# Kernel tuning notes

Hardware: AMD Instinct MI355X
Metric: run time of the kernel (lower is better)

The kernel has to match this reference:

```python
import jax, jax.numpy as jnp
import numpy as np

COMPRESSION = 2

def setup_inputs() -> dict:
    key = jax.random.key(0)
    k = jax.random.split(key, 5)
    B, H, W, C, Ci = 8, 56, 56, 256, 128
    return {
        "x": jax.random.normal(k[0], (B, H, W, C), dtype=jnp.float32),
        "w_theta": jax.random.normal(k[1], (C, Ci), dtype=jnp.float32) * (2.0 / C) ** 0.5,
        "w_phi": jax.random.normal(k[2], (C, Ci), dtype=jnp.float32) * (2.0 / C) ** 0.5,
        "w_g": jax.random.normal(k[3], (C, Ci), dtype=jnp.float32) * (2.0 / C) ** 0.5,
        "w_final": jax.random.normal(k[4], (Ci, C), dtype=jnp.float32) * (2.0 / Ci) ** 0.5,
    }

def _maxpool1d(z, pool):
    # z: [B, N, Ci]; non-overlapping max pool along N (Keras MaxPool1D default stride=pool)
    B, N, Ci = z.shape
    return z[:, : (N // pool) * pool].reshape(B, N // pool, pool, Ci).max(axis=2)

def reference(x, w_theta, w_phi, w_g, w_final):
    B, H, W, C = x.shape
    Ci = w_theta.shape[1]
    N = H * W
    xf = x.reshape(B, N, C)
    # 1x1 convs == per-position matmuls
    theta = xf @ w_theta                      # [B, N, Ci]
    phi = _maxpool1d(xf @ w_phi, COMPRESSION)  # [B, N/2, Ci]
    g = _maxpool1d(xf @ w_g, COMPRESSION)      # [B, N/2, Ci]
    f = jnp.einsum('bnc,bmc->bnm', theta, phi)  # [B, N, N/2]
    f = jax.nn.softmax(f, axis=-1)
    y = jnp.einsum('bnm,bmc->bnc', f, g)        # [B, N, Ci]
    z = y @ w_final                              # [B, N, C]
    return x + z.reshape(B, H, W, C)
```

## Files before the change

### kernel.cpp

```cpp
#include <hip/hip_runtime.h>

typedef _Float16 f16x8 __attribute__((ext_vector_type(8)));
typedef short s16x4 __attribute__((ext_vector_type(4)));
typedef float f32x4 __attribute__((ext_vector_type(4)));

#define MFMA_K32(a, b, c) __builtin_amdgcn_mfma_f32_16x16x32_f16(a, b, c, 0, 0, 0)
#define MFMA_BF(a, b, c)  __builtin_amdgcn_mfma_f32_16x16x16bf16_1k(a, b, c, 0, 0, 0)


__device__ __forceinline__ f16x8 ld8f(const float* __restrict__ p) {
    f32x4 a = *(const f32x4*)p;
    f32x4 b = *(const f32x4*)(p + 4);
    f16x8 r;
    r[0] = (_Float16)a[0]; r[1] = (_Float16)a[1];
    r[2] = (_Float16)a[2]; r[3] = (_Float16)a[3];
    r[4] = (_Float16)b[0]; r[5] = (_Float16)b[1];
    r[6] = (_Float16)b[2]; r[7] = (_Float16)b[3];
    return r;
}
__device__ __forceinline__ unsigned f2bf_rne(float f) {
    unsigned u = __float_as_uint(f);
    return (u + 0x7FFFu + ((u >> 16) & 1u)) >> 16;
}
__device__ __forceinline__ int bfpack_rtz(float lo, float hi) {
    return (int)((__float_as_uint(hi) & 0xFFFF0000u) | (__float_as_uint(lo) >> 16));
}

__global__ void k_prep(const float* __restrict__ wt, const float* __restrict__ wp,
                       const float* __restrict__ wg, const float* __restrict__ wf,
                       _Float16* __restrict__ wt_f, _Float16* __restrict__ wf_f) {
    int i = blockIdx.x * 256 + threadIdx.x;
    int w = i >> 15, idx = i & 32767;
    if (w < 3) {
        const float* src = (w == 0) ? wt : (w == 1) ? wp : wg;
        int k = idx >> 7, n = idx & 127;
        int ct = n >> 4, tt = n & 15, kc = k >> 5, qq = (k >> 3) & 3, jj = k & 7;
        wt_f[((w * 8 + ct) * 8 + kc) * 512 + (qq * 16 + tt) * 8 + jj] = (_Float16)src[idx];
    } else {
        int k = idx >> 8, n = idx & 255;
        int cb = n >> 7, ct = (n >> 4) & 7, tt = n & 15;
        int kc = k >> 5, qq = (k >> 3) & 3, jj = k & 7;
        wf_f[((cb * 8 + ct) * 4 + kc) * 512 + (qq * 16 + tt) * 8 + jj] = (_Float16)wf[idx];
    }
}

__global__ __launch_bounds__(128) void k_proj(
    const float* __restrict__ x,
    const _Float16* __restrict__ wt_f,
    _Float16* __restrict__ theta_f,
    _Float16* __restrict__ phi_f,
    short* __restrict__ g_f)
{
    const int r0   = blockIdx.x * 32;
    const int wave = threadIdx.x >> 6;
    const int lane = threadIdx.x & 63;
    const int q = lane >> 4, t = lane & 15;

    const int mrow = r0 + wave * 16 + t;
    f16x8 af[8];
#pragma unroll
    for (int kc = 0; kc < 8; ++kc)
        af[kc] = ld8f(x + mrow * 256 + kc * 32 + q * 8);

    const f32x4 zero = {0.f, 0.f, 0.f, 0.f};
    f32x4 acc[3][8];
#pragma unroll
    for (int w = 0; w < 3; ++w)
#pragma unroll
        for (int ct = 0; ct < 8; ++ct) acc[w][ct] = zero;

#pragma unroll
    for (int w = 0; w < 3; ++w)
#pragma unroll
        for (int ct = 0; ct < 8; ++ct) {
            const _Float16* Wc = wt_f + ((w * 8 + ct) * 8) * 512 + lane * 8;
#pragma unroll
            for (int kc = 0; kc < 8; ++kc)
                acc[w][ct] = MFMA_K32(af[kc], *(const f16x8*)(Wc + kc * 512), acc[w][ct]);
        }

    _Float16* tb = theta_f + (blockIdx.x * 2 + wave) * 2048;
#pragma unroll
    for (int ct = 0; ct < 8; ++ct) {
        const int off = (ct >> 1) * 512 + ((ct & 1) * 2 + (t >> 3)) * 128 + (t & 7);
#pragma unroll
        for (int r = 0; r < 4; ++r)
            tb[off + (q * 4 + r) * 8] = (_Float16)acc[0][ct][r];
    }

    const int b     = blockIdx.x / 98;
    const int mIdx  = blockIdx.x % 98;
    const int chunk = mIdx >> 1;
    const int h     = mIdx & 1;
    const int ttp   = wave * 8 + q * 2;

    _Float16* pcb = phi_f + (b * 49 + chunk) * 4096;
#pragma unroll
    for (int ct = 0; ct < 8; ++ct) {
        const int kc = ct >> 1;
        const int qq = (ct & 1) * 2 + (t >> 3);
        const int j  = t & 7;
        const int off = (h * 4 + kc) * 512 + (qq * 16 + ttp) * 8 + j;
        pcb[off]     = (_Float16)fmaxf(acc[1][ct][0], acc[1][ct][1]);
        pcb[off + 8] = (_Float16)fmaxf(acc[1][ct][2], acc[1][ct][3]);
    }

    short* gcb = g_f + (b * 49 + chunk) * 4096;
    const int qv  = wave * 2 + (q >> 1);
    const int jj0 = (q & 1) * 2;
#pragma unroll
    for (int ct = 0; ct < 8; ++ct) {
        unsigned lo = f2bf_rne(fmaxf(acc[2][ct][0], acc[2][ct][1]));
        unsigned hi = f2bf_rne(fmaxf(acc[2][ct][2], acc[2][ct][3]));
        *(unsigned*)(gcb + ct * 512 + (qv * 16 + t) * 8 + h * 4 + jj0) = lo | (hi << 16);
    }
}

__global__ __launch_bounds__(256) void k_attn(
    const _Float16* __restrict__ theta_f,
    const _Float16* __restrict__ phi_f,
    const short* __restrict__ g_f,
    _Float16* __restrict__ y_f)
{
    const int blk  = blockIdx.x;
    const int b    = blk & 7;
    const int blkm = blk >> 3;
    const int wave = threadIdx.x >> 6;
    const int lane = threadIdx.x & 63;
    const int q = lane >> 4, t = lane & 15;

    __shared__ __align__(16) _Float16 kv[2][8192];

    const int tIdx = b * 196 + blkm * 4 + wave;
    const _Float16* ph = phi_f + b * 200704;
    const _Float16* gt = (const _Float16*)(g_f + b * 200704);

    f16x8 qf[4];
#pragma unroll
    for (int kc = 0; kc < 4; ++kc)
        qf[kc] = *(const f16x8*)(theta_f + tIdx * 2048 + kc * 512 + lane * 8);

    const f32x4 zero = {0.f, 0.f, 0.f, 0.f};
    f32x4 o[8];
#pragma unroll
    for (int ct = 0; ct < 8; ++ct) o[ct] = zero;
    float lsum = 0.f;
    const float L2E = 1.44269504f, SHIFT = 104.0f;

    const _Float16* src0 = (wave < 2) ? (ph + wave * 2048) : (gt + (wave - 2) * 2048);
    const int doff = wave * 2048;

    f16x8 sr[4];
#pragma unroll
    for (int j = 0; j < 4; ++j)
        sr[j] = *(const f16x8*)(src0 + j * 512 + lane * 8);
#pragma unroll
    for (int j = 0; j < 4; ++j)
        *(f16x8*)(&kv[0][doff + j * 512 + lane * 8]) = sr[j];
    __syncthreads();

    for (int i = 0; i < 49; ++i) {
        if (i + 1 < 49) {
            const _Float16* s = src0 + (i + 1) * 4096;
#pragma unroll
            for (int j = 0; j < 4; ++j)
                sr[j] = *(const f16x8*)(s + j * 512 + lane * 8);
        }

        const _Float16* buf = &kv[i & 1][0];
        f32x4 st0 = zero, st1 = zero;
#pragma unroll
        for (int kc = 0; kc < 4; ++kc) {
            f16x8 a0 = *(const f16x8*)(buf + kc * 512 + lane * 8);
            f16x8 a1 = *(const f16x8*)(buf + (4 + kc) * 512 + lane * 8);
            st0 = MFMA_K32(a0, qf[kc], st0);
            st1 = MFMA_K32(a1, qf[kc], st1);
        }

        f32x4 p0, p1;
#pragma unroll
        for (int r = 0; r < 4; ++r) {
            p0[r] = exp2f(st0[r] * L2E - SHIFT);
            p1[r] = exp2f(st1[r] * L2E - SHIFT);
        }
        lsum += ((p0[0] + p0[1]) + (p0[2] + p0[3]))
              + ((p1[0] + p1[1]) + (p1[2] + p1[3]));
        union { int i2[2]; s16x4 v; } u0, u1;
        u0.i2[0] = bfpack_rtz(p0[0], p0[1]);
        u0.i2[1] = bfpack_rtz(p0[2], p0[3]);
        u1.i2[0] = bfpack_rtz(p1[0], p1[1]);
        u1.i2[1] = bfpack_rtz(p1[2], p1[3]);

#pragma unroll
        for (int ct = 0; ct < 8; ++ct) {
            union { f16x8 f; s16x4 s[2]; } uv;
            uv.f = *(const f16x8*)(buf + 4096 + ct * 512 + lane * 8);
            o[ct] = MFMA_BF(u0.v, uv.s[0], o[ct]);
            o[ct] = MFMA_BF(u1.v, uv.s[1], o[ct]);
        }

        if (i + 1 < 49) {
            _Float16* d = &kv[(i + 1) & 1][doff];
#pragma unroll
            for (int j = 0; j < 4; ++j)
                *(f16x8*)(d + j * 512 + lane * 8) = sr[j];
        }
        __syncthreads();
    }

    float lf = lsum;
    lf += __shfl_xor(lf, 16);
    lf += __shfl_xor(lf, 32);
    float inv[4];
#pragma unroll
    for (int r = 0; r < 4; ++r) inv[r] = 1.0f / __shfl(lf, q * 4 + r);

    _Float16* yb = y_f + tIdx * 2048;
#pragma unroll
    for (int ct = 0; ct < 8; ++ct) {
        const int off = (ct >> 1) * 512 + (2 * (ct & 1) + (t >> 3)) * 128 + (t & 7);
#pragma unroll
        for (int r = 0; r < 4; ++r)
            yb[off + (4 * q + r) * 8] = (_Float16)(o[ct][r] * inv[r]);
    }
}

__global__ __launch_bounds__(256) void k_final(
    const _Float16* __restrict__ y_f,
    const _Float16* __restrict__ wf_f,
    const float* __restrict__ x,
    float* __restrict__ out)
{
    const int r0   = blockIdx.x * 64;
    const int cb   = blockIdx.y;
    const int wave = threadIdx.x >> 6;
    const int lane = threadIdx.x & 63;
    const int q = lane >> 4, t = lane & 15;

    __shared__ float t_lds[4][16][132];

    const int tile = blockIdx.x * 4 + wave;
    f16x8 af[4];
#pragma unroll
    for (int kc = 0; kc < 4; ++kc)
        af[kc] = *(const f16x8*)(y_f + tile * 2048 + kc * 512 + lane * 8);

    const f32x4 zero = {0.f, 0.f, 0.f, 0.f};
    f32x4 acc[8];
#pragma unroll
    for (int ct = 0; ct < 8; ++ct) acc[ct] = zero;
#pragma unroll
    for (int ct = 0; ct < 8; ++ct) {
        const _Float16* Wc = wf_f + ((cb * 8 + ct) * 4) * 512 + lane * 8;
#pragma unroll
        for (int kc = 0; kc < 4; ++kc)
            acc[ct] = MFMA_K32(af[kc], *(const f16x8*)(Wc + kc * 512), acc[ct]);
    }

#pragma unroll
    for (int ct = 0; ct < 8; ++ct)
#pragma unroll
        for (int r = 0; r < 4; ++r)
            t_lds[wave][q * 4 + r][ct * 16 + t] = acc[ct][r];

    const int R0 = r0 + wave * 16;
#pragma unroll
    for (int p = 0; p < 4; ++p) {
        const int rr = p * 4 + q;
        const int c  = t * 8;
        f32x4 v0 = *(const f32x4*)&t_lds[wave][rr][c];
        f32x4 v1 = *(const f32x4*)&t_lds[wave][rr][c + 4];
        const float* xp = x + (R0 + rr) * 256 + cb * 128 + c;
        float* op = out + (R0 + rr) * 256 + cb * 128 + c;
        v0 += *(const f32x4*)xp;
        v1 += *(const f32x4*)(xp + 4);
        *(f32x4*)op = v0;
        *(f32x4*)(op + 4) = v1;
    }
}

extern "C" void kernel_launch(void* const* d_in, const int* in_sizes, int n_in,
                              void* d_out, int out_size, void* d_ws, size_t ws_size,
                              hipStream_t stream) {
    const float* x  = (const float*)d_in[0];
    const float* wt = (const float*)d_in[1];
    const float* wp = (const float*)d_in[2];
    const float* wg = (const float*)d_in[3];
    const float* wf = (const float*)d_in[4];
    float* out = (float*)d_out;

    _Float16* ws      = (_Float16*)d_ws;
    _Float16* wt_f    = ws;
    _Float16* wf_f    = ws + 98304;
    _Float16* theta_f = ws + 131072;
    _Float16* phi_f   = ws + 3342336;
    short*    g_f     = (short*)(ws + 4947968);
    _Float16* y_f     = ws + 6553600;

    k_prep <<<dim3(512),    256, 0, stream>>>(wt, wp, wg, wf, wt_f, wf_f);
    k_proj <<<dim3(784),    128, 0, stream>>>(x, wt_f, theta_f, phi_f, g_f);
    k_attn <<<dim3(392),    256, 0, stream>>>(theta_f, phi_f, g_f, y_f);
    k_final<<<dim3(392, 2), 256, 0, stream>>>(y_f, wf_f, x, out);
}
```

Before: 159.8 us.

## Process two query tiles per wave in attention kernel with 128-thread blocks

Each attention block now runs two waves instead of four, and each wave computes two 16-row query tiles. Every K/V fragment read from LDS is therefore reused across two MFMA chains, which halves LDS read traffic per unit of output and lengthens the independent MFMA stream. The cost is roughly twice the accumulator registers per wave, twice the global loads per thread for K/V staging, and fewer waves per block to hide latency. This may reduce occupancy.

```diff
diff --git a/kernel.cpp b/kernel.cpp
--- a/kernel.cpp
+++ b/kernel.cpp
@@ -116,7 +116,7 @@
     }
 }
 
-__global__ __launch_bounds__(256) void k_attn(
+__global__ __launch_bounds__(128) void k_attn(
     const _Float16* __restrict__ theta_f,
     const _Float16* __restrict__ phi_f,
     const short* __restrict__ g_f,
@@ -131,31 +131,35 @@
 
     __shared__ __align__(16) _Float16 kv[2][8192];
 
-    const int tIdx = b * 196 + blkm * 4 + wave;
+    const int tIdx0 = b * 196 + blkm * 4 + wave * 2;
     const _Float16* ph = phi_f + b * 200704;
     const _Float16* gt = (const _Float16*)(g_f + b * 200704);
 
-    f16x8 qf[4];
-#pragma unroll
-    for (int kc = 0; kc < 4; ++kc)
-        qf[kc] = *(const f16x8*)(theta_f + tIdx * 2048 + kc * 512 + lane * 8);
+    f16x8 qf[2][4];
+#pragma unroll
+    for (int mt = 0; mt < 2; ++mt)
+#pragma unroll
+        for (int kc = 0; kc < 4; ++kc)
+            qf[mt][kc] = *(const f16x8*)(theta_f + (tIdx0 + mt) * 2048 + kc * 512 + lane * 8);
 
     const f32x4 zero = {0.f, 0.f, 0.f, 0.f};
-    f32x4 o[8];
-#pragma unroll
-    for (int ct = 0; ct < 8; ++ct) o[ct] = zero;
-    float lsum = 0.f;
+    f32x4 o[2][8];
+#pragma unroll
+    for (int mt = 0; mt < 2; ++mt)
+#pragma unroll
+        for (int ct = 0; ct < 8; ++ct) o[mt][ct] = zero;
+    float lsum[2] = {0.f, 0.f};
     const float L2E = 1.44269504f, SHIFT = 104.0f;
 
-    const _Float16* src0 = (wave < 2) ? (ph + wave * 2048) : (gt + (wave - 2) * 2048);
-    const int doff = wave * 2048;
-
-    f16x8 sr[4];
-#pragma unroll
-    for (int j = 0; j < 4; ++j)
+    const _Float16* src0 = (wave == 0) ? ph : gt;
+    const int doff = wave * 4096;
+
+    f16x8 sr[8];
+#pragma unroll
+    for (int j = 0; j < 8; ++j)
         sr[j] = *(const f16x8*)(src0 + j * 512 + lane * 8);
 #pragma unroll
-    for (int j = 0; j < 4; ++j)
+    for (int j = 0; j < 8; ++j)
         *(f16x8*)(&kv[0][doff + j * 512 + lane * 8]) = sr[j];
     __syncthreads();
 
@@ -163,65 +167,80 @@
         if (i + 1 < 49) {
             const _Float16* s = src0 + (i + 1) * 4096;
 #pragma unroll
-            for (int j = 0; j < 4; ++j)
+            for (int j = 0; j < 8; ++j)
                 sr[j] = *(const f16x8*)(s + j * 512 + lane * 8);
         }
 
         const _Float16* buf = &kv[i & 1][0];
-        f32x4 st0 = zero, st1 = zero;
+        f32x4 st00 = zero, st01 = zero, st10 = zero, st11 = zero;
 #pragma unroll
         for (int kc = 0; kc < 4; ++kc) {
             f16x8 a0 = *(const f16x8*)(buf + kc * 512 + lane * 8);
             f16x8 a1 = *(const f16x8*)(buf + (4 + kc) * 512 + lane * 8);
-            st0 = MFMA_K32(a0, qf[kc], st0);
-            st1 = MFMA_K32(a1, qf[kc], st1);
-        }
-
-        f32x4 p0, p1;
-#pragma unroll
-        for (int r = 0; r < 4; ++r) {
-            p0[r] = exp2f(st0[r] * L2E - SHIFT);
-            p1[r] = exp2f(st1[r] * L2E - SHIFT);
-        }
-        lsum += ((p0[0] + p0[1]) + (p0[2] + p0[3]))
-              + ((p1[0] + p1[1]) + (p1[2] + p1[3]));
-        union { int i2[2]; s16x4 v; } u0, u1;
-        u0.i2[0] = bfpack_rtz(p0[0], p0[1]);
-        u0.i2[1] = bfpack_rtz(p0[2], p0[3]);
-        u1.i2[0] = bfpack_rtz(p1[0], p1[1]);
-        u1.i2[1] = bfpack_rtz(p1[2], p1[3]);
+            st00 = MFMA_K32(a0, qf[0][kc], st00);
+            st10 = MFMA_K32(a1, qf[0][kc], st10);
+            st01 = MFMA_K32(a0, qf[1][kc], st01);
+            st11 = MFMA_K32(a1, qf[1][kc], st11);
+        }
+
+        s16x4 pa[2][2];
+#pragma unroll
+        for (int mt = 0; mt < 2; ++mt) {
+            f32x4 s0 = mt ? st01 : st00;
+            f32x4 s1 = mt ? st11 : st10;
+            f32x4 p0, p1;
+#pragma unroll
+            for (int r = 0; r < 4; ++r) {
+                p0[r] = exp2f(s0[r] * L2E - SHIFT);
+                p1[r] = exp2f(s1[r] * L2E - SHIFT);
+            }
+            lsum[mt] += ((p0[0] + p0[1]) + (p0[2] + p0[3]))
+                      + ((p1[0] + p1[1]) + (p1[2] + p1[3]));
+            union { int i2[2]; s16x4 v; } u0, u1;
+            u0.i2[0] = bfpack_rtz(p0[0], p0[1]);
+            u0.i2[1] = bfpack_rtz(p0[2], p0[3]);
+            u1.i2[0] = bfpack_rtz(p1[0], p1[1]);
+            u1.i2[1] = bfpack_rtz(p1[2], p1[3]);
+            pa[mt][0] = u0.v;
+            pa[mt][1] = u1.v;
+        }
 
 #pragma unroll
         for (int ct = 0; ct < 8; ++ct) {
             union { f16x8 f; s16x4 s[2]; } uv;
             uv.f = *(const f16x8*)(buf + 4096 + ct * 512 + lane * 8);
-            o[ct] = MFMA_BF(u0.v, uv.s[0], o[ct]);
-            o[ct] = MFMA_BF(u1.v, uv.s[1], o[ct]);
+            o[0][ct] = MFMA_BF(pa[0][0], uv.s[0], o[0][ct]);
+            o[0][ct] = MFMA_BF(pa[0][1], uv.s[1], o[0][ct]);
+            o[1][ct] = MFMA_BF(pa[1][0], uv.s[0], o[1][ct]);
+            o[1][ct] = MFMA_BF(pa[1][1], uv.s[1], o[1][ct]);
         }
 
         if (i + 1 < 49) {
             _Float16* d = &kv[(i + 1) & 1][doff];
 #pragma unroll
-            for (int j = 0; j < 4; ++j)
+            for (int j = 0; j < 8; ++j)
                 *(f16x8*)(d + j * 512 + lane * 8) = sr[j];
         }
         __syncthreads();
     }
 
-    float lf = lsum;
-    lf += __shfl_xor(lf, 16);
-    lf += __shfl_xor(lf, 32);
-    float inv[4];
-#pragma unroll
-    for (int r = 0; r < 4; ++r) inv[r] = 1.0f / __shfl(lf, q * 4 + r);
-
-    _Float16* yb = y_f + tIdx * 2048;
-#pragma unroll
-    for (int ct = 0; ct < 8; ++ct) {
-        const int off = (ct >> 1) * 512 + (2 * (ct & 1) + (t >> 3)) * 128 + (t & 7);
-#pragma unroll
-        for (int r = 0; r < 4; ++r)
-            yb[off + (4 * q + r) * 8] = (_Float16)(o[ct][r] * inv[r]);
+#pragma unroll
+    for (int mt = 0; mt < 2; ++mt) {
+        float lf = lsum[mt];
+        lf += __shfl_xor(lf, 16);
+        lf += __shfl_xor(lf, 32);
+        float inv[4];
+#pragma unroll
+        for (int r = 0; r < 4; ++r) inv[r] = 1.0f / __shfl(lf, q * 4 + r);
+
+        _Float16* yb = y_f + (tIdx0 + mt) * 2048;
+#pragma unroll
+        for (int ct = 0; ct < 8; ++ct) {
+            const int off = (ct >> 1) * 512 + (2 * (ct & 1) + (t >> 3)) * 128 + (t & 7);
+#pragma unroll
+            for (int r = 0; r < 4; ++r)
+                yb[off + (4 * q + r) * 8] = (_Float16)(o[mt][ct][r] * inv[r]);
+        }
     }
 }
 
@@ -299,6 +318,6 @@
 
     k_prep <<<dim3(512),    256, 0, stream>>>(wt, wp, wg, wf, wt_f, wf_f);
     k_proj <<<dim3(784),    128, 0, stream>>>(x, wt_f, theta_f, phi_f, g_f);
-    k_attn <<<dim3(392),    256, 0, stream>>>(theta_f, phi_f, g_f, y_f);
+    k_attn <<<dim3(392),    128, 0, stream>>>(theta_f, phi_f, g_f, y_f);
     k_final<<<dim3(392, 2), 256, 0, stream>>>(y_f, wf_f, x, out);
 }
```

New measurement: 185.6 us. 1.16x slower.
